# Kernel tuning notes

Measured on AMD Instinct MI355X. Metric: run time of the kernel, lower is better.

Reference implementation:

```python
import jax, jax.numpy as jnp
import numpy as np

B, T, C = 8, 4096, 1024
NH = 64          # module sets self.n_head = dim_head = 64
HD = C // NH     # 16


def setup_inputs() -> dict:
    key = jax.random.key(0)
    ks = jax.random.split(key, 9)
    s = 1.0 / np.sqrt(C).astype(np.float32)
    x = jax.random.normal(ks[0], (B, T, C), jnp.float32)
    Wq = jax.random.normal(ks[1], (C, C), jnp.float32) * s
    bq = jax.random.normal(ks[2], (C,), jnp.float32) * 0.01
    Wk = jax.random.normal(ks[3], (C, C), jnp.float32) * s
    bk = jax.random.normal(ks[4], (C,), jnp.float32) * 0.01
    Wv = jax.random.normal(ks[5], (C, C), jnp.float32) * s
    bv = jax.random.normal(ks[6], (C,), jnp.float32) * 0.01
    Wp = jax.random.normal(ks[7], (C, C), jnp.float32) * s
    bp = jax.random.normal(ks[8], (C,), jnp.float32) * 0.01
    return {"x": x, "Wq": Wq, "bq": bq, "Wk": Wk, "bk": bk,
            "Wv": Wv, "bv": bv, "Wp": Wp, "bp": bp}


def _heads(t):
    # [B, T, C] -> [B, NH, T, HD]
    return t.reshape(B, T, NH, HD).transpose(0, 2, 1, 3)


def reference(x, Wq, bq, Wk, bk, Wv, bv, Wp, bp):
    # self-attention path: y = x; kv_mask=None (masked path is unreachable in source)
    q = _heads(x @ Wq.T + bq)
    k = _heads(x @ Wk.T + bk)
    v = _heads(x @ Wv.T + bv)
    q = jax.nn.softmax(q, axis=-1)
    k = jax.nn.softmax(k, axis=-1)
    k_cumsum = k.sum(axis=2, keepdims=True)               # [B, NH, 1, HD]
    D_inv = 1.0 / (q * k_cumsum).sum(axis=-1, keepdims=True)  # [B, NH, T, 1]
    context = jnp.einsum('bhtd,bhte->bhde', k, v)          # [B, NH, HD, HD]
    y = jnp.einsum('bhtd,bhde->bhte', q, context) * D_inv  # [B, NH, T, HD]
    y = y.transpose(0, 2, 1, 3).reshape(B, T, C)           # b h n d -> b n (h d)
    return y @ Wp.T + bp
```

## Files before the change

kernel.cpp:

```cpp
#include <hip/hip_runtime.h>
#include <stdint.h>


typedef __attribute__((ext_vector_type(8))) __bf16 bf16x8;
typedef __attribute__((ext_vector_type(4))) float f32x4;
typedef __attribute__((ext_vector_type(4))) unsigned int u32x4;
typedef __attribute__((ext_vector_type(4))) unsigned short u16x4;

#define AS1 __attribute__((address_space(1)))
#define AS3 __attribute__((address_space(3)))

__device__ __forceinline__ unsigned short f2bf(float f) {
  unsigned int u = __builtin_bit_cast(unsigned int, f);
  u += 0x7FFFu + ((u >> 16) & 1u);
  return (unsigned short)(u >> 16);
}

__device__ __forceinline__ void gl_lds16(const unsigned short* g, unsigned short* l) {
  __builtin_amdgcn_global_load_lds((const AS1 unsigned int*)g, (AS3 unsigned int*)l, 16, 0, 0);
}

__global__ __launch_bounds__(256)
void cvt_x(const float* __restrict__ src, unsigned short* __restrict__ dst, int n4) {
  int i = blockIdx.x * blockDim.x + threadIdx.x;
  const int stride = gridDim.x * blockDim.x;
  for (; i < n4; i += stride) {
    f32x4 v = *(const f32x4*)(src + (size_t)i * 4);
    u16x4 o;
    o.x = f2bf(v.x); o.y = f2bf(v.y); o.z = f2bf(v.z); o.w = f2bf(v.w);
    *(u16x4*)(dst + (size_t)i * 4) = o;
  }
}

__global__ __launch_bounds__(256)
void cvt_w(const float* __restrict__ w0, const float* __restrict__ w1,
           const float* __restrict__ w2, const float* __restrict__ w3,
           unsigned short* __restrict__ dst) {
  const int g = blockIdx.x * 256 + threadIdx.x;
  const int w = g >> 17;
  const int r = g & 131071;
  const int f = r >> 6;
  const int l = r & 63;
  const int n = (f >> 5) * 16 + (l & 15);
  const int k = (f & 31) * 32 + (l >> 4) * 8;
  const float* ws[4] = {w0, w1, w2, w3};
  const float* src = ws[w] + (size_t)n * 1024 + k;
  f32x4 v0 = *(const f32x4*)src;
  f32x4 v1 = *(const f32x4*)(src + 4);
  u16x4 a, b;
  a.x = f2bf(v0.x); a.y = f2bf(v0.y); a.z = f2bf(v0.z); a.w = f2bf(v0.w);
  b.x = f2bf(v1.x); b.y = f2bf(v1.y); b.z = f2bf(v1.z); b.w = f2bf(v1.w);
  unsigned short* o = dst + (size_t)g * 8;
  *(u16x4*)o = a;
  *(u16x4*)(o + 4) = b;
}

template<int KIND>
__global__ __launch_bounds__(256, 3)
void gemm_pipe(const unsigned short* __restrict__ A,
               const unsigned short* __restrict__ Wf,
               const float* __restrict__ b0, const float* __restrict__ b1,
               const float* __restrict__ b2,
               unsigned short* __restrict__ oq, unsigned short* __restrict__ okT,
               unsigned short* __restrict__ ovT, float* __restrict__ of)
{
  __shared__ __align__(16) unsigned short lds[24576];

  const int tid  = threadIdx.x;
  const int lane = tid & 63;
  const int wid  = tid >> 6;

  const int flat  = blockIdx.x;
  const int xcd   = flat & 7;
  const int i     = flat >> 3;
  const int bcg   = i >> 8;
  const int r     = i & 255;
  const int panel = r >> 3;
  const int c     = r & 7;
  const int brow  = (xcd * 32 + panel) * 128;
  const int bcol  = (bcg * 8 + c) * 128;

  const int srow = wid * 16 + (lane >> 2);
  const int scol = ((lane & 3) ^ ((lane >> 3) & 3)) << 3;
  const unsigned short* a_src = A + (size_t)(brow + srow) * 1024 + scol;
  unsigned short* Ldst = lds + wid * 512;

  const int wm = (wid >> 1) * 64;
  const int wn = (wid & 1) * 64;
  const int fr = lane & 15;
  const int fg = lane >> 4;
  const int aoff = (wm + fr) * 32 + ((fg ^ ((fr >> 1) & 3)) << 3);

  const unsigned short* wfp = Wf + ((size_t)((bcol + wn) >> 4) * 32) * 512 + lane * 8;

  const f32x4 fz = {0.f, 0.f, 0.f, 0.f};
  f32x4 acc[4][4];
  #pragma unroll
  for (int mt = 0; mt < 4; ++mt)
    #pragma unroll
    for (int nt = 0; nt < 4; ++nt) acc[mt][nt] = fz;

  auto stage = [&](int T, int sb) {
    unsigned short* d = Ldst + sb * 8192;
    const unsigned short* g = a_src + T * 64;
    gl_lds16(g,              d);
    gl_lds16(g + 65536,      d + 2048);
    gl_lds16(g + 32,         d + 4096);
    gl_lds16(g + 65536 + 32, d + 6144);
  };
  auto loadB = [&](int k32, bf16x8 (&dst)[4]) {
    #pragma unroll
    for (int nt = 0; nt < 4; ++nt)
      dst[nt] = __builtin_bit_cast(bf16x8,
        *(const u32x4*)(wfp + (size_t)k32 * 512 + (size_t)nt * 16384));
  };

  bf16x8 bEven[4], bOdd[4];

  stage(0, 0); stage(1, 1);
  loadB(0, bEven);
  asm volatile("s_waitcnt vmcnt(8)" ::: "memory");
  __builtin_amdgcn_sched_barrier(0);
  __builtin_amdgcn_s_barrier();

  for (int T = 0; T < 16; ++T) {
    const unsigned short* Lb = lds + (T % 3) * 8192;
    bf16x8 af[8];
    #pragma unroll
    for (int mt = 0; mt < 4; ++mt) {
      af[mt]     = __builtin_bit_cast(bf16x8, *(const u32x4*)&Lb[aoff + mt * 512]);
      af[4 + mt] = __builtin_bit_cast(bf16x8, *(const u32x4*)&Lb[4096 + aoff + mt * 512]);
    }
    asm volatile("s_waitcnt lgkmcnt(0)" ::: "memory");
    __builtin_amdgcn_sched_barrier(0);
    if (T + 2 < 16) stage(T + 2, (T + 2) % 3);
    loadB(2 * T + 1, bOdd);
    if (T <= 13)      asm volatile("s_waitcnt vmcnt(8)" ::: "memory");
    else              asm volatile("s_waitcnt vmcnt(4)" ::: "memory");
    __builtin_amdgcn_sched_barrier(0);
    if (T < 15) __builtin_amdgcn_s_barrier();

    __builtin_amdgcn_s_setprio(1);
    #pragma unroll
    for (int mt = 0; mt < 4; ++mt)
      #pragma unroll
      for (int nt = 0; nt < 4; ++nt)
        acc[mt][nt] = __builtin_amdgcn_mfma_f32_16x16x32_bf16(af[mt], bEven[nt], acc[mt][nt], 0, 0, 0);
    __builtin_amdgcn_s_setprio(0);

    if (T <= 14) loadB(2 * T + 2, bEven);
    if (T <= 13)      asm volatile("s_waitcnt vmcnt(8)" ::: "memory");
    else if (T == 14) asm volatile("s_waitcnt vmcnt(4)" ::: "memory");
    else              asm volatile("s_waitcnt vmcnt(0)" ::: "memory");
    __builtin_amdgcn_sched_barrier(0);

    __builtin_amdgcn_s_setprio(1);
    #pragma unroll
    for (int mt = 0; mt < 4; ++mt)
      #pragma unroll
      for (int nt = 0; nt < 4; ++nt)
        acc[mt][nt] = __builtin_amdgcn_mfma_f32_16x16x32_bf16(af[4 + mt], bOdd[nt], acc[mt][nt], 0, 0, 0);
    __builtin_amdgcn_s_setprio(0);
  }

  const int sec = (KIND == 0) ? (bcol >> 10) : 0;
  const float* bias = (KIND == 1) ? b0 : (sec == 0 ? b0 : (sec == 1 ? b1 : b2));

  #pragma unroll
  for (int nt = 0; nt < 4; ++nt) {
    const int n_glob = bcol + wn + nt * 16 + fr;
    const int nn = (KIND == 0) ? (n_glob & 1023) : n_glob;
    const float bv = bias[nn];
    #pragma unroll
    for (int mt = 0; mt < 4; ++mt) {
      const int m0 = brow + wm + mt * 16 + fg * 4;
      float vals[4];
      #pragma unroll
      for (int r2 = 0; r2 < 4; ++r2) vals[r2] = acc[mt][nt][r2] + bv;

      if (KIND == 0 && sec <= 1) {
        #pragma unroll
        for (int r2 = 0; r2 < 4; ++r2) {
          float e = __expf(vals[r2]);
          float sm = e;
          #pragma unroll
          for (int s = 1; s < 16; s <<= 1) sm += __shfl_xor(sm, s, 64);
          vals[r2] = e * __builtin_amdgcn_rcpf(sm);
        }
      }

      if (KIND == 1) {
        #pragma unroll
        for (int r2 = 0; r2 < 4; ++r2)
          of[(size_t)(m0 + r2) * 1024 + n_glob] = vals[r2];
      } else if (sec == 0) {
        #pragma unroll
        for (int r2 = 0; r2 < 4; ++r2)
          oq[(size_t)(m0 + r2) * 1024 + nn] = f2bf(vals[r2]);
      } else {
        unsigned short* o = (sec == 1) ? okT : ovT;
        const int bb = m0 >> 12;
        const int t0 = m0 & 4095;
        const int hh = nn >> 4;
        const int dd = nn & 15;
        u16x4 pk;
        pk.x = f2bf(vals[0]); pk.y = f2bf(vals[1]);
        pk.z = f2bf(vals[2]); pk.w = f2bf(vals[3]);
        *(u16x4*)&o[(((size_t)bb * 64 + hh) * 16 + dd) * 4096 + t0] = pk;
      }
    }
  }
}

__global__ __launch_bounds__(256)
void attn_kernel(const unsigned short* __restrict__ qb,
                 const unsigned short* __restrict__ kT,
                 const unsigned short* __restrict__ vT,
                 unsigned short* __restrict__ yb)
{
  const int pair = blockIdx.x;
  const int b    = pair >> 5;
  const int hp   = pair & 31;
  const int tid  = threadIdx.x;
  const int lane = tid & 63;
  const int wid  = tid >> 6;
  const int fr   = lane & 15;
  const int fg   = lane >> 4;

  const unsigned short* kT0 = kT + ((size_t)(b * 64 + hp * 2) * 16) * 4096;
  const unsigned short* vT0 = vT + ((size_t)(b * 64 + hp * 2) * 16) * 4096;
  const unsigned short* kT1 = kT0 + 16 * 4096;
  const unsigned short* vT1 = vT0 + 16 * 4096;

  const u32x4 uz = {0u, 0u, 0u, 0u};
  const f32x4 fz = {0.f, 0.f, 0.f, 0.f};
  const u32x4 uo = {0x3F803F80u, 0x3F803F80u, 0x3F803F80u, 0x3F803F80u};
  const bf16x8 ones = __builtin_bit_cast(bf16x8, uo);

  f32x4 cctx0 = fz, ckc0 = fz, cctx1 = fz, ckc1 = fz;
  #pragma unroll 2
  for (int t0 = wid * 1024; t0 < (wid + 1) * 1024; t0 += 32) {
    const size_t off = (size_t)fr * 4096 + t0 + fg * 8;
    bf16x8 ak0 = __builtin_bit_cast(bf16x8, *(const u32x4*)&kT0[off]);
    bf16x8 bv0 = __builtin_bit_cast(bf16x8, *(const u32x4*)&vT0[off]);
    bf16x8 ak1 = __builtin_bit_cast(bf16x8, *(const u32x4*)&kT1[off]);
    bf16x8 bv1 = __builtin_bit_cast(bf16x8, *(const u32x4*)&vT1[off]);
    cctx0 = __builtin_amdgcn_mfma_f32_16x16x32_bf16(ak0, bv0, cctx0, 0, 0, 0);
    ckc0  = __builtin_amdgcn_mfma_f32_16x16x32_bf16(ak0, ones, ckc0, 0, 0, 0);
    cctx1 = __builtin_amdgcn_mfma_f32_16x16x32_bf16(ak1, bv1, cctx1, 0, 0, 0);
    ckc1  = __builtin_amdgcn_mfma_f32_16x16x32_bf16(ak1, ones, ckc1, 0, 0, 0);
  }

  __shared__ float red[4][2][16][16];
  __shared__ float kcr[4][2][16];
  __shared__ float ctxf[2][16][16];
  __shared__ float kcf[2][16];

  #pragma unroll
  for (int r = 0; r < 4; ++r) {
    red[wid][0][fg * 4 + r][fr] = cctx0[r];
    red[wid][1][fg * 4 + r][fr] = cctx1[r];
  }
  if (fr == 0) {
    #pragma unroll
    for (int r = 0; r < 4; ++r) {
      kcr[wid][0][fg * 4 + r] = ckc0[r];
      kcr[wid][1][fg * 4 + r] = ckc1[r];
    }
  }
  __syncthreads();
  {
    const int d = (tid >> 4) & 15, e = tid & 15;
    #pragma unroll
    for (int hh = 0; hh < 2; ++hh)
      ctxf[hh][d][e] = red[0][hh][d][e] + red[1][hh][d][e] + red[2][hh][d][e] + red[3][hh][d][e];
    if (tid < 32) {
      const int hh = tid >> 4, dd = tid & 15;
      kcf[hh][dd] = kcr[0][hh][dd] + kcr[1][hh][dd] + kcr[2][hh][dd] + kcr[3][hh][dd];
    }
  }
  __syncthreads();

  bf16x8 bctx0 = __builtin_bit_cast(bf16x8, uz);
  bf16x8 bctx1 = __builtin_bit_cast(bf16x8, uz);
  bf16x8 bkc0  = __builtin_bit_cast(bf16x8, uz);
  bf16x8 bkc1  = __builtin_bit_cast(bf16x8, uz);
  if (fg < 2) {
    #pragma unroll
    for (int j = 0; j < 8; ++j) {
      const int d = fg * 8 + j;
      bctx0[j] = (__bf16)ctxf[0][d][fr];
      bkc0[j]  = (__bf16)kcf[0][d];
    }
  } else {
    #pragma unroll
    for (int j = 0; j < 8; ++j) {
      const int d = (fg - 2) * 8 + j;
      bctx1[j] = (__bf16)ctxf[1][d][fr];
      bkc1[j]  = (__bf16)kcf[1][d];
    }
  }

  const size_t cbase = (size_t)b * 4096 * 1024 + (size_t)hp * 32;

  for (int step = 0; step < 64; ++step) {
    const int t0 = step * 64 + wid * 16;
    bf16x8 af = __builtin_bit_cast(bf16x8,
        *(const u32x4*)&qb[cbase + (size_t)(t0 + fr) * 1024 + fg * 8]);
    f32x4 cy0 = __builtin_amdgcn_mfma_f32_16x16x32_bf16(af, bctx0, fz, 0, 0, 0);
    f32x4 cy1 = __builtin_amdgcn_mfma_f32_16x16x32_bf16(af, bctx1, fz, 0, 0, 0);
    f32x4 cd0 = __builtin_amdgcn_mfma_f32_16x16x32_bf16(af, bkc0,  fz, 0, 0, 0);
    f32x4 cd1 = __builtin_amdgcn_mfma_f32_16x16x32_bf16(af, bkc1,  fz, 0, 0, 0);
    #pragma unroll
    for (int r = 0; r < 4; ++r) {
      const int t = t0 + fg * 4 + r;
      const size_t o = cbase + (size_t)t * 1024;
      yb[o + fr]      = f2bf(cy0[r] * __builtin_amdgcn_rcpf(cd0[r]));
      yb[o + 16 + fr] = f2bf(cy1[r] * __builtin_amdgcn_rcpf(cd1[r]));
    }
  }
}

extern "C" void kernel_launch(void* const* d_in, const int* in_sizes, int n_in,
                              void* d_out, int out_size, void* d_ws, size_t ws_size,
                              hipStream_t stream)
{
  (void)in_sizes; (void)n_in; (void)out_size; (void)ws_size;
  const float* x  = (const float*)d_in[0];
  const float* Wq = (const float*)d_in[1];
  const float* bq = (const float*)d_in[2];
  const float* Wk = (const float*)d_in[3];
  const float* bk = (const float*)d_in[4];
  const float* Wv = (const float*)d_in[5];
  const float* bv = (const float*)d_in[6];
  const float* Wp = (const float*)d_in[7];
  const float* bp = (const float*)d_in[8];

  char* ws = (char*)d_ws;
  unsigned short* xb  = (unsigned short*)(ws);
  unsigned short* wb  = (unsigned short*)(ws + 67108864);
  unsigned short* qb  = (unsigned short*)(ws + 75497472);
  unsigned short* kTb = (unsigned short*)(ws + 142606336);
  unsigned short* vTb = (unsigned short*)(ws + 209715200);

  cvt_x<<<2048, 256, 0, stream>>>(x, xb, 33554432 / 4);
  cvt_w<<<2048, 256, 0, stream>>>(Wq, Wk, Wv, Wp, wb);

  gemm_pipe<0><<<6144, 256, 0, stream>>>(xb, wb, bq, bk, bv, qb, kTb, vTb, nullptr);

  attn_kernel<<<256, 256, 0, stream>>>(qb, kTb, vTb, xb );

  gemm_pipe<1><<<2048, 256, 0, stream>>>(xb , wb + 3145728, bp, bp, bp,
                                         nullptr, nullptr, nullptr, (float*)d_out);
}
```

Baseline: 453.5 us.

## Prefetch next A fragments across iterations and merge conversion kernels

The GEMM main loop now loads the first half of the next K-tile's A fragments from LDS during the current iteration, double-buffering them in registers across an unrolled-by-two loop. The second-half fragment read is issued alongside the B global loads, and the barrier and waitcnt placement are reordered so LDS reads overlap MFMA work. The x and weight fp32-to-bf16 conversions are merged into one launch to remove a kernel launch gap. The change adds register pressure, and the reordered waits and barriers risk LDS hazards if the counts are wrong.

```diff
diff --git a/kernel.cpp b/kernel.cpp
--- a/kernel.cpp
+++ b/kernel.cpp
@@ -21,38 +21,39 @@
 }
 
 __global__ __launch_bounds__(256)
-void cvt_x(const float* __restrict__ src, unsigned short* __restrict__ dst, int n4) {
-  int i = blockIdx.x * blockDim.x + threadIdx.x;
-  const int stride = gridDim.x * blockDim.x;
-  for (; i < n4; i += stride) {
-    f32x4 v = *(const f32x4*)(src + (size_t)i * 4);
-    u16x4 o;
-    o.x = f2bf(v.x); o.y = f2bf(v.y); o.z = f2bf(v.z); o.w = f2bf(v.w);
-    *(u16x4*)(dst + (size_t)i * 4) = o;
-  }
-}
-
-__global__ __launch_bounds__(256)
-void cvt_w(const float* __restrict__ w0, const float* __restrict__ w1,
-           const float* __restrict__ w2, const float* __restrict__ w3,
-           unsigned short* __restrict__ dst) {
-  const int g = blockIdx.x * 256 + threadIdx.x;
-  const int w = g >> 17;
-  const int r = g & 131071;
-  const int f = r >> 6;
-  const int l = r & 63;
-  const int n = (f >> 5) * 16 + (l & 15);
-  const int k = (f & 31) * 32 + (l >> 4) * 8;
-  const float* ws[4] = {w0, w1, w2, w3};
-  const float* src = ws[w] + (size_t)n * 1024 + k;
-  f32x4 v0 = *(const f32x4*)src;
-  f32x4 v1 = *(const f32x4*)(src + 4);
-  u16x4 a, b;
-  a.x = f2bf(v0.x); a.y = f2bf(v0.y); a.z = f2bf(v0.z); a.w = f2bf(v0.w);
-  b.x = f2bf(v1.x); b.y = f2bf(v1.y); b.z = f2bf(v1.z); b.w = f2bf(v1.w);
-  unsigned short* o = dst + (size_t)g * 8;
-  *(u16x4*)o = a;
-  *(u16x4*)(o + 4) = b;
+void cvt_all(const float* __restrict__ x,
+             const float* __restrict__ w0, const float* __restrict__ w1,
+             const float* __restrict__ w2, const float* __restrict__ w3,
+             unsigned short* __restrict__ xb, unsigned short* __restrict__ wb) {
+  const int blk = blockIdx.x;
+  if (blk < 2048) {
+    int i = blk * 256 + threadIdx.x;
+    #pragma unroll 4
+    for (; i < 8388608; i += 524288) {
+      f32x4 v = *(const f32x4*)(x + (size_t)i * 4);
+      u16x4 o;
+      o.x = f2bf(v.x); o.y = f2bf(v.y); o.z = f2bf(v.z); o.w = f2bf(v.w);
+      *(u16x4*)(xb + (size_t)i * 4) = o;
+    }
+  } else {
+    const int g = (blk - 2048) * 256 + threadIdx.x;
+    const int w = g >> 17;
+    const int r = g & 131071;
+    const int f = r >> 6;
+    const int l = r & 63;
+    const int n = (f >> 5) * 16 + (l & 15);
+    const int k = (f & 31) * 32 + (l >> 4) * 8;
+    const float* ws[4] = {w0, w1, w2, w3};
+    const float* src = ws[w] + (size_t)n * 1024 + k;
+    f32x4 v0 = *(const f32x4*)src;
+    f32x4 v1 = *(const f32x4*)(src + 4);
+    u16x4 a, b;
+    a.x = f2bf(v0.x); a.y = f2bf(v0.y); a.z = f2bf(v0.z); a.w = f2bf(v0.w);
+    b.x = f2bf(v1.x); b.y = f2bf(v1.y); b.z = f2bf(v1.z); b.w = f2bf(v1.w);
+    unsigned short* o = wb + (size_t)g * 8;
+    *(u16x4*)o = a;
+    *(u16x4*)(o + 4) = b;
+  }
 }
 
 template<int KIND>
@@ -116,51 +117,59 @@
   };
 
   bf16x8 bEven[4], bOdd[4];
+  bf16x8 af0A[4], af0B[4], af1[4];
 
   stage(0, 0); stage(1, 1);
   loadB(0, bEven);
   asm volatile("s_waitcnt vmcnt(8)" ::: "memory");
   __builtin_amdgcn_sched_barrier(0);
   __builtin_amdgcn_s_barrier();
-
-  for (int T = 0; T < 16; ++T) {
-    const unsigned short* Lb = lds + (T % 3) * 8192;
-    bf16x8 af[8];
-    #pragma unroll
-    for (int mt = 0; mt < 4; ++mt) {
-      af[mt]     = __builtin_bit_cast(bf16x8, *(const u32x4*)&Lb[aoff + mt * 512]);
-      af[4 + mt] = __builtin_bit_cast(bf16x8, *(const u32x4*)&Lb[4096 + aoff + mt * 512]);
-    }
-    asm volatile("s_waitcnt lgkmcnt(0)" ::: "memory");
-    __builtin_amdgcn_sched_barrier(0);
-    if (T + 2 < 16) stage(T + 2, (T + 2) % 3);
+  #pragma unroll
+  for (int mt = 0; mt < 4; ++mt)
+    af0A[mt] = __builtin_bit_cast(bf16x8, *(const u32x4*)&lds[aoff + mt * 512]);
+
+  auto body = [&](int T, bf16x8 (&af0c)[4], bf16x8 (&af0n)[4]) {
     loadB(2 * T + 1, bOdd);
-    if (T <= 13)      asm volatile("s_waitcnt vmcnt(8)" ::: "memory");
-    else              asm volatile("s_waitcnt vmcnt(4)" ::: "memory");
+    {
+      const unsigned short* Lb1 = lds + (T % 3) * 8192 + 4096;
+      #pragma unroll
+      for (int mt = 0; mt < 4; ++mt)
+        af1[mt] = __builtin_bit_cast(bf16x8, *(const u32x4*)&Lb1[aoff + mt * 512]);
+    }
+    asm volatile("s_waitcnt vmcnt(4)" ::: "memory");
     __builtin_amdgcn_sched_barrier(0);
     if (T < 15) __builtin_amdgcn_s_barrier();
-
+    if (T + 2 < 16) stage(T + 2, (T + 2) % 3);
+    if (T < 15) {
+      const unsigned short* Lb0 = lds + ((T + 1) % 3) * 8192;
+      #pragma unroll
+      for (int mt = 0; mt < 4; ++mt)
+        af0n[mt] = __builtin_bit_cast(bf16x8, *(const u32x4*)&Lb0[aoff + mt * 512]);
+    }
     __builtin_amdgcn_s_setprio(1);
     #pragma unroll
     for (int mt = 0; mt < 4; ++mt)
       #pragma unroll
       for (int nt = 0; nt < 4; ++nt)
-        acc[mt][nt] = __builtin_amdgcn_mfma_f32_16x16x32_bf16(af[mt], bEven[nt], acc[mt][nt], 0, 0, 0);
+        acc[mt][nt] = __builtin_amdgcn_mfma_f32_16x16x32_bf16(af0c[mt], bEven[nt], acc[mt][nt], 0, 0, 0);
     __builtin_amdgcn_s_setprio(0);
-
-    if (T <= 14) loadB(2 * T + 2, bEven);
+    if (T < 15) loadB(2 * T + 2, bEven);
     if (T <= 13)      asm volatile("s_waitcnt vmcnt(8)" ::: "memory");
     else if (T == 14) asm volatile("s_waitcnt vmcnt(4)" ::: "memory");
     else              asm volatile("s_waitcnt vmcnt(0)" ::: "memory");
     __builtin_amdgcn_sched_barrier(0);
-
     __builtin_amdgcn_s_setprio(1);
     #pragma unroll
     for (int mt = 0; mt < 4; ++mt)
       #pragma unroll
       for (int nt = 0; nt < 4; ++nt)
-        acc[mt][nt] = __builtin_amdgcn_mfma_f32_16x16x32_bf16(af[4 + mt], bOdd[nt], acc[mt][nt], 0, 0, 0);
+        acc[mt][nt] = __builtin_amdgcn_mfma_f32_16x16x32_bf16(af1[mt], bOdd[nt], acc[mt][nt], 0, 0, 0);
     __builtin_amdgcn_s_setprio(0);
+  };
+
+  for (int T = 0; T < 16; T += 2) {
+    body(T,     af0A, af0B);
+    body(T + 1, af0B, af0A);
   }
 
   const int sec = (KIND == 0) ? (bcol >> 10) : 0;
@@ -343,8 +352,7 @@
   unsigned short* kTb = (unsigned short*)(ws + 142606336);
   unsigned short* vTb = (unsigned short*)(ws + 209715200);
 
-  cvt_x<<<2048, 256, 0, stream>>>(x, xb, 33554432 / 4);
-  cvt_w<<<2048, 256, 0, stream>>>(Wq, Wk, Wv, Wp, wb);
+  cvt_all<<<4096, 256, 0, stream>>>(x, Wq, Wk, Wv, Wp, xb, wb);
 
   gemm_pipe<0><<<6144, 256, 0, stream>>>(xb, wb, bq, bk, bv, qb, kTb, vTb, nullptr);
 
```

After: 451.5 us. Within noise of the previous version (-0.4%).
